# Performance work log

Measured on AMD Instinct MI355X. Metric: run time of the kernel, lower is better.

## Reference

```python
import jax, jax.numpy as jnp
import numpy as np

D_MODEL = 1024
NUM_HEADS = 16
D_K = D_MODEL // NUM_HEADS


def setup_inputs() -> dict:
    key = jax.random.key(0)
    ks = jax.random.split(key, 11)
    B, S, D = 4, 2048, D_MODEL
    scale = 1.0 / np.sqrt(D)
    return {
        "Q": jax.random.normal(ks[0], (B, S, D), jnp.float32),
        "K": jax.random.normal(ks[1], (B, S, D), jnp.float32),
        "V": jax.random.normal(ks[2], (B, S, D), jnp.float32),
        "Wq": jax.random.normal(ks[3], (D, D), jnp.float32) * scale,
        "bq": jnp.zeros((D,), jnp.float32),
        "Wk": jax.random.normal(ks[4], (D, D), jnp.float32) * scale,
        "bk": jnp.zeros((D,), jnp.float32),
        "Wv": jax.random.normal(ks[5], (D, D), jnp.float32) * scale,
        "bv": jnp.zeros((D,), jnp.float32),
        "Wo": jax.random.normal(ks[6], (D, D), jnp.float32) * scale,
        "bo": jnp.zeros((D,), jnp.float32),
    }


def reference(Q, K, V, Wq, bq, Wk, bk, Wv, bv, Wo, bo):
    B, S, D = Q.shape
    H, Dk = NUM_HEADS, D_K
    # projections: [B,S,D] -> [B,H,S,Dk]
    def proj(x, W, b):
        y = jnp.einsum('bsd,de->bse', x, W.T) + b  # torch Linear: x @ W.T + b
        return y.reshape(B, -1, H, Dk).transpose(0, 2, 1, 3)
    q = proj(Q, Wq, bq)
    k = proj(K, Wk, bk)
    v = proj(V, Wv, bv)
    scores = jnp.einsum('bhqd,bhkd->bhqk', q, k) / np.sqrt(Dk)  # [B,H,S,S]
    attn = jax.nn.softmax(scores, axis=-1)
    out = jnp.einsum('bhqk,bhkd->bhqd', attn, v)  # [B,H,S,Dk]
    out = out.transpose(0, 2, 1, 3).reshape(B, -1, D)
    return jnp.einsum('bsd,de->bse', out, Wo.T) + bo
```

## Files before the change

### kernel.cpp

```cpp
#include <hip/hip_runtime.h>


typedef __bf16 bhalf_t;
typedef __attribute__((ext_vector_type(8)))  __bf16 bf16x8;
typedef __attribute__((ext_vector_type(4)))  __bf16 bf16x4;
typedef __attribute__((ext_vector_type(4)))  float  f32x4;
typedef __attribute__((ext_vector_type(16))) float  f32x16;

typedef __attribute__((address_space(1))) void gvoid_t;
typedef __attribute__((address_space(3))) void lvoid_t;
#define GLD16(g, l) __builtin_amdgcn_global_load_lds((const gvoid_t*)(g), (lvoid_t*)(l), 16, 0, 0)

__global__ __launch_bounds__(256) void cvt_all(
    const float* __restrict__ Q, const float* __restrict__ Kin, const float* __restrict__ V,
    const float* __restrict__ Wq, const float* __restrict__ Wk, const float* __restrict__ Wv,
    const float* __restrict__ Wo,
    bhalf_t* __restrict__ Qb, bhalf_t* __restrict__ Kb, bhalf_t* __restrict__ Vb,
    bhalf_t* __restrict__ Wqb, bhalf_t* __restrict__ Wkb, bhalf_t* __restrict__ Wvb,
    bhalf_t* __restrict__ Wob)
{
  size_t t = (size_t)blockIdx.x * 256 + threadIdx.x;
  const float* src; bhalf_t* dst;
  if (t < 2097152)      { src = Q;   dst = Qb; }
  else if (t < 4194304) { src = Kin; dst = Kb; t -= 2097152; }
  else if (t < 6291456) { src = V;   dst = Vb; t -= 4194304; }
  else {
    t -= 6291456;
    int w = (int)(t >> 18); t &= 262143;
    src = (w == 0) ? Wq  : (w == 1) ? Wk  : (w == 2) ? Wv  : Wo;
    dst = (w == 0) ? Wqb : (w == 1) ? Wkb : (w == 2) ? Wvb : Wob;
  }
  float4 f = ((const float4*)src)[t];
  bf16x4 o;
  o.x = (bhalf_t)f.x; o.y = (bhalf_t)f.y; o.z = (bhalf_t)f.z; o.w = (bhalf_t)f.w;
  ((bf16x4*)dst)[t] = o;
}

__device__ __forceinline__ void gemm_core_128_swz(
    const bhalf_t* __restrict__ A, const bhalf_t* __restrict__ B,
    int bm, int bn, bhalf_t* As, bhalf_t* Bs, f32x4 acc[4][4])
{
  const int tid = threadIdx.x, lane = tid & 63, wave = tid >> 6;
  const int wm = wave >> 1, wn = wave & 1;
  const int quad = lane >> 4, tn = lane & 15;

  const int u    = (lane & 7) ^ (lane >> 3);
  const int roff = (lane >> 3) + 64 * (u >> 2);
  const int gk   = (u & 3) * 8;

  const bhalf_t* Ag0 = A + (size_t)(bm * 128 + wave * 8 + roff) * 1024 + gk;
  const bhalf_t* Ag1 = A + (size_t)(bm * 128 + (wave + 4) * 8 + roff) * 1024 + gk;
  const bhalf_t* Bg0 = B + (size_t)(bn * 128 + wave * 8 + roff) * 1024 + gk;
  const bhalf_t* Bg1 = B + (size_t)(bn * 128 + (wave + 4) * 8 + roff) * 1024 + gk;
  bhalf_t* Ad0 = As + wave * 512;  bhalf_t* Ad1 = As + (wave + 4) * 512;
  bhalf_t* Bd0 = Bs + wave * 512;  bhalf_t* Bd1 = Bs + (wave + 4) * 512;

  const int aswz = ((wm * 4 + quad) ^ (tn & 7)) * 8;
  const int bswz = ((wn * 4 + quad) ^ (tn & 7)) * 8;

  for (int k0 = 0; k0 < 1024; k0 += 32) {
    GLD16(Ag0 + k0, Ad0);
    GLD16(Ag1 + k0, Ad1);
    GLD16(Bg0 + k0, Bd0);
    GLD16(Bg1 + k0, Bd1);
    __syncthreads();
    bf16x8 af[4], bfr[4];
#pragma unroll
    for (int i = 0; i < 4; ++i)
      af[i] = *(const bf16x8*)(As + (i * 16 + tn) * 64 + aswz);
#pragma unroll
    for (int j = 0; j < 4; ++j)
      bfr[j] = *(const bf16x8*)(Bs + (j * 16 + tn) * 64 + bswz);
#pragma unroll
    for (int i = 0; i < 4; ++i)
#pragma unroll
      for (int j = 0; j < 4; ++j)
        acc[i][j] = __builtin_amdgcn_mfma_f32_16x16x32_bf16(af[i], bfr[j], acc[i][j], 0, 0, 0);
    __syncthreads();
  }
}

__global__ __launch_bounds__(256) void proj_gemm(
    const bhalf_t* __restrict__ Qb, const bhalf_t* __restrict__ Kb, const bhalf_t* __restrict__ Vb,
    const bhalf_t* __restrict__ Wqb, const bhalf_t* __restrict__ Wkb, const bhalf_t* __restrict__ Wvb,
    const float* __restrict__ bq, const float* __restrict__ bk, const float* __restrict__ bv,
    bhalf_t* __restrict__ qo, bhalf_t* __restrict__ ko, bhalf_t* __restrict__ vto)
{
  __shared__ bhalf_t As[4096];
  __shared__ bhalf_t Bs[4096];
  const int seg = blockIdx.x >> 9;
  const int idx = blockIdx.x & 511;
  const int bm = idx & 63, bn = idx >> 6;

  const bhalf_t *A, *Bw; const float* bias; bhalf_t* out; float scale; int mode;
  if (seg == 0)      { A = Qb; Bw = Wqb; bias = bq; out = qo;  scale = 0.18033688f; mode = 0; }
  else if (seg == 1) { A = Kb; Bw = Wkb; bias = bk; out = ko;  scale = 1.0f;        mode = 0; }
  else               { A = Vb; Bw = Wvb; bias = bv; out = vto; scale = 1.0f;        mode = 1; }

  f32x4 acc[4][4];
#pragma unroll
  for (int i = 0; i < 4; ++i)
#pragma unroll
    for (int j = 0; j < 4; ++j)
      acc[i][j] = (f32x4){0.f, 0.f, 0.f, 0.f};

  gemm_core_128_swz(A, Bw, bm, bn, As, Bs, acc);

  const int lane = threadIdx.x & 63, wave = threadIdx.x >> 6;
  const int wm = wave >> 1, wn = wave & 1, quad = lane >> 4, tn = lane & 15;
#pragma unroll
  for (int i = 0; i < 4; ++i)
#pragma unroll
    for (int j = 0; j < 4; ++j) {
      const int n = bn * 128 + wn * 64 + j * 16 + tn;
      const float bsv = bias[n];
      const int h = n >> 6, dk = n & 63;
#pragma unroll
      for (int r = 0; r < 4; ++r) {
        const int m = bm * 128 + wm * 64 + i * 16 + quad * 4 + r;
        const int b = m >> 11, s = m & 2047;
        const float v = (acc[i][j][r] + bsv) * scale;
        size_t addr;
        if (mode == 0) addr = (((size_t)(b * 16 + h)) * 2048 + s) * 64 + dk;
        else {
          const int s2 = (s & ~12) | ((s & 4) << 1) | ((s & 8) >> 1);
          addr = (((size_t)(b * 16 + h)) * 64 + dk) * 2048 + s2;
        }
        out[addr] = (bhalf_t)v;
      }
    }
}

__global__ __launch_bounds__(256) void out_gemm(
    const bhalf_t* __restrict__ A, const bhalf_t* __restrict__ Bw,
    const float* __restrict__ bias, float* __restrict__ Cout)
{
  __shared__ bhalf_t As[4096];
  __shared__ bhalf_t Bs[4096];
  const int bm = blockIdx.x & 63, bn = blockIdx.x >> 6;

  f32x4 acc[4][4];
#pragma unroll
  for (int i = 0; i < 4; ++i)
#pragma unroll
    for (int j = 0; j < 4; ++j)
      acc[i][j] = (f32x4){0.f, 0.f, 0.f, 0.f};

  gemm_core_128_swz(A, Bw, bm, bn, As, Bs, acc);

  const int lane = threadIdx.x & 63, wave = threadIdx.x >> 6;
  const int wm = wave >> 1, wn = wave & 1, quad = lane >> 4, tn = lane & 15;
#pragma unroll
  for (int i = 0; i < 4; ++i)
#pragma unroll
    for (int j = 0; j < 4; ++j) {
      const int n = bn * 128 + wn * 64 + j * 16 + tn;
      const float bsv = bias[n];
#pragma unroll
      for (int r = 0; r < 4; ++r) {
        const int m = bm * 128 + wm * 64 + i * 16 + quad * 4 + r;
        Cout[(size_t)m * 1024 + n] = acc[i][j][r] + bsv;
      }
    }
}

__global__ __launch_bounds__(256, 2) void attn_kernel(
    const bhalf_t* __restrict__ qp, const bhalf_t* __restrict__ kp,
    const bhalf_t* __restrict__ vtp, bhalf_t* __restrict__ outp)
{
  __shared__ bhalf_t Klds[4096];
  __shared__ bhalf_t Vtlds[4096];

  const int tid = threadIdx.x, lane = tid & 63, wave = tid >> 6;
  const int q31 = lane & 31, h = lane >> 5;
  const int bh = blockIdx.y, qt = blockIdx.x;

  const bhalf_t* qbase = qp + (((size_t)bh * 2048) + qt * 256 + wave * 64 + q31) * 64;
  bf16x8 qf[2][4];
#pragma unroll
  for (int qs = 0; qs < 2; ++qs)
#pragma unroll
    for (int ks = 0; ks < 4; ++ks)
      qf[qs][ks] = *(const bf16x8*)(qbase + qs * 32 * 64 + ks * 16 + h * 8);

  f32x16 Ot[2][2];
#pragma unroll
  for (int qs = 0; qs < 2; ++qs)
#pragma unroll
    for (int dd = 0; dd < 2; ++dd)
#pragma unroll
      for (int i = 0; i < 16; ++i) Ot[qs][dd][i] = 0.f;
  float Lp[2] = {0.f, 0.f};

  const bhalf_t* kbase  = kp  + (size_t)bh * 2048 * 64;
  const bhalf_t* vtbase = vtp + (size_t)bh * 64 * 2048;

  const int rloc = lane >> 3;
  const int cg8  = ((lane & 7) ^ rloc) * 8;
  const int q7 = q31 & 7;

  for (int kv0 = 0; kv0 < 2048; kv0 += 64) {
#pragma unroll
    for (int i = 0; i < 2; ++i) {
      const int r0 = (wave * 2 + i) * 8;
      GLD16(kbase + (size_t)(kv0 + r0 + rloc) * 64 + cg8, Klds + r0 * 64);
      GLD16(vtbase + (size_t)(r0 + rloc) * 2048 + kv0 + cg8, Vtlds + r0 * 64);
    }
    __syncthreads();

    bf16x8 pb[2][4];
#pragma unroll
    for (int mb = 0; mb < 2; ++mb) {
      bf16x8 ka[4];
#pragma unroll
      for (int ks = 0; ks < 4; ++ks)
        ka[ks] = *(const bf16x8*)(Klds + (mb * 32 + q31) * 64 + ((2 * ks + h) ^ q7) * 8);
#pragma unroll
      for (int qs = 0; qs < 2; ++qs) {
        f32x16 S;
#pragma unroll
        for (int i = 0; i < 16; ++i) S[i] = 0.f;
#pragma unroll
        for (int ks = 0; ks < 4; ++ks)
          S = __builtin_amdgcn_mfma_f32_32x32x16_bf16(ka[ks], qf[qs][ks], S, 0, 0, 0);
        float ls = 0.f;
#pragma unroll
        for (int half = 0; half < 2; ++half) {
          bf16x8 pk;
#pragma unroll
          for (int j = 0; j < 8; ++j) {
            const float e = __builtin_amdgcn_exp2f(S[half * 8 + j]);
            ls += e;
            pk[j] = (bhalf_t)e;
          }
          pb[qs][mb * 2 + half] = pk;
        }
        Lp[qs] += ls;
      }
    }

#pragma unroll
    for (int dd = 0; dd < 2; ++dd)
#pragma unroll
      for (int kb = 0; kb < 4; ++kb) {
        const bf16x8 va = *(const bf16x8*)(Vtlds + (dd * 32 + q31) * 64 + ((2 * kb + h) ^ q7) * 8);
#pragma unroll
        for (int qs = 0; qs < 2; ++qs)
          Ot[qs][dd] = __builtin_amdgcn_mfma_f32_32x32x16_bf16(va, pb[qs][kb], Ot[qs][dd], 0, 0, 0);
      }
    __syncthreads();
  }

  const int b = bh >> 4, hh = bh & 15;
#pragma unroll
  for (int qs = 0; qs < 2; ++qs) {
    const float Lt = Lp[qs] + __shfl_xor(Lp[qs], 32, 64);
    const float linv = 1.0f / Lt;
    const int s = qt * 256 + wave * 64 + qs * 32 + q31;
    bhalf_t* ob = outp + ((size_t)(b * 2048 + s)) * 1024 + hh * 64;
#pragma unroll
    for (int dd = 0; dd < 2; ++dd)
#pragma unroll
      for (int g = 0; g < 4; ++g) {
        bf16x4 o;
        o.x = (bhalf_t)(Ot[qs][dd][4 * g + 0] * linv);
        o.y = (bhalf_t)(Ot[qs][dd][4 * g + 1] * linv);
        o.z = (bhalf_t)(Ot[qs][dd][4 * g + 2] * linv);
        o.w = (bhalf_t)(Ot[qs][dd][4 * g + 3] * linv);
        *(bf16x4*)(ob + dd * 32 + g * 8 + h * 4) = o;
      }
  }
}

extern "C" void kernel_launch(void* const* d_in, const int* in_sizes, int n_in,
                              void* d_out, int out_size, void* d_ws, size_t ws_size,
                              hipStream_t stream)
{
  const float* Q  = (const float*)d_in[0];
  const float* K  = (const float*)d_in[1];
  const float* V  = (const float*)d_in[2];
  const float* Wq = (const float*)d_in[3];
  const float* bq = (const float*)d_in[4];
  const float* Wk = (const float*)d_in[5];
  const float* bk = (const float*)d_in[6];
  const float* Wv = (const float*)d_in[7];
  const float* bv = (const float*)d_in[8];
  const float* Wo = (const float*)d_in[9];
  const float* bo = (const float*)d_in[10];

  char* ws = (char*)d_ws;
  const size_t SZ = 8192ull * 1024 * 2;
  const size_t WZ = 1024ull * 1024 * 2;
  bhalf_t* Qb   = (bhalf_t*)(ws);
  bhalf_t* Kb   = (bhalf_t*)(ws + SZ);
  bhalf_t* Vb   = (bhalf_t*)(ws + 2 * SZ);
  bhalf_t* Wqb  = (bhalf_t*)(ws + 3 * SZ);
  bhalf_t* Wkb  = (bhalf_t*)(ws + 3 * SZ + WZ);
  bhalf_t* Wvb  = (bhalf_t*)(ws + 3 * SZ + 2 * WZ);
  bhalf_t* Wob  = (bhalf_t*)(ws + 3 * SZ + 3 * WZ);
  bhalf_t* q_p  = (bhalf_t*)(ws + 3 * SZ + 4 * WZ);
  bhalf_t* k_p  = (bhalf_t*)(ws + 4 * SZ + 4 * WZ);
  bhalf_t* vt_p = (bhalf_t*)(ws + 5 * SZ + 4 * WZ);
  bhalf_t* attn_o = Qb;

  cvt_all<<<28672, 256, 0, stream>>>(Q, K, V, Wq, Wk, Wv, Wo,
                                     Qb, Kb, Vb, Wqb, Wkb, Wvb, Wob);
  proj_gemm<<<1536, 256, 0, stream>>>(Qb, Kb, Vb, Wqb, Wkb, Wvb,
                                      bq, bk, bv, q_p, k_p, vt_p);
  attn_kernel<<<dim3(8, 64), 256, 0, stream>>>(q_p, k_p, vt_p, attn_o);
  out_gemm<<<512, 256, 0, stream>>>(attn_o, Wob, bo, (float*)d_out);
}
```

Measured before the change: 334.8 us.

## Double-buffer attention K/V tiles, widen projection GEMM K-tile, reorder attention grid

The attention kernel now keeps two LDS buffers for K and V^T and prefetches the next 64-key tile while computing on the current one. This removes the barrier wait on loads at the top of every iteration. The projection GEMM is inlined with a 64-wide K step, which halves the number of barrier round trips per tile but doubles its LDS footprint. The attention grid is transposed so that consecutive blocks walk across batch-heads rather than query tiles, which changes L2 locality for K/V. Together these raise LDS use per block, which may affect occupancy.

```diff
diff --git a/kernel.cpp b/kernel.cpp
--- a/kernel.cpp
+++ b/kernel.cpp
@@ -86,8 +86,8 @@
     const float* __restrict__ bq, const float* __restrict__ bk, const float* __restrict__ bv,
     bhalf_t* __restrict__ qo, bhalf_t* __restrict__ ko, bhalf_t* __restrict__ vto)
 {
-  __shared__ bhalf_t As[4096];
-  __shared__ bhalf_t Bs[4096];
+  __shared__ bhalf_t As[8192];
+  __shared__ bhalf_t Bs[8192];
   const int seg = blockIdx.x >> 9;
   const int idx = blockIdx.x & 511;
   const int bm = idx & 63, bn = idx >> 6;
@@ -97,6 +97,19 @@
   else if (seg == 1) { A = Kb; Bw = Wkb; bias = bk; out = ko;  scale = 1.0f;        mode = 0; }
   else               { A = Vb; Bw = Wvb; bias = bv; out = vto; scale = 1.0f;        mode = 1; }
 
+  const int tid = threadIdx.x, lane = tid & 63, wave = tid >> 6;
+  const int wm = wave >> 1, wn = wave & 1;
+  const int quad = lane >> 4, tn = lane & 15;
+  const int u = (lane & 7) ^ (lane >> 3);
+
+  const bhalf_t* Agp[4]; const bhalf_t* Bgp[4];
+#pragma unroll
+  for (int g = 0; g < 4; ++g) {
+    const int row = g * 32 + wave * 8 + (lane >> 3);
+    Agp[g] = A  + (size_t)(bm * 128 + row) * 1024 + u * 8;
+    Bgp[g] = Bw + (size_t)(bn * 128 + row) * 1024 + u * 8;
+  }
+
   f32x4 acc[4][4];
 #pragma unroll
   for (int i = 0; i < 4; ++i)
@@ -104,20 +117,45 @@
     for (int j = 0; j < 4; ++j)
       acc[i][j] = (f32x4){0.f, 0.f, 0.f, 0.f};
 
-  gemm_core_128_swz(A, Bw, bm, bn, As, Bs, acc);
-
-  const int lane = threadIdx.x & 63, wave = threadIdx.x >> 6;
-  const int wm = wave >> 1, wn = wave & 1, quad = lane >> 4, tn = lane & 15;
+  for (int k0 = 0; k0 < 1024; k0 += 64) {
+#pragma unroll
+    for (int g = 0; g < 4; ++g) {
+      GLD16(Agp[g] + k0, As + g * 2048 + wave * 512);
+      GLD16(Bgp[g] + k0, Bs + g * 2048 + wave * 512);
+    }
+    __syncthreads();
+#pragma unroll
+    for (int kk = 0; kk < 2; ++kk) {
+      bf16x8 af[4], bfr[4];
+#pragma unroll
+      for (int i = 0; i < 4; ++i)
+        af[i] = *(const bf16x8*)(As + (wm * 64 + i * 16 + tn) * 64
+                                    + (((kk * 4 + quad) ^ (tn & 7)) * 8));
+#pragma unroll
+      for (int j = 0; j < 4; ++j)
+        bfr[j] = *(const bf16x8*)(Bs + (wn * 64 + j * 16 + tn) * 64
+                                     + (((kk * 4 + quad) ^ (tn & 7)) * 8));
+#pragma unroll
+      for (int i = 0; i < 4; ++i)
+#pragma unroll
+        for (int j = 0; j < 4; ++j)
+          acc[i][j] = __builtin_amdgcn_mfma_f32_16x16x32_bf16(af[i], bfr[j], acc[i][j], 0, 0, 0);
+    }
+    __syncthreads();
+  }
+
+  const int lane2 = threadIdx.x & 63, wave2 = threadIdx.x >> 6;
+  const int wm2 = wave2 >> 1, wn2 = wave2 & 1, quad2 = lane2 >> 4, tn2 = lane2 & 15;
 #pragma unroll
   for (int i = 0; i < 4; ++i)
 #pragma unroll
     for (int j = 0; j < 4; ++j) {
-      const int n = bn * 128 + wn * 64 + j * 16 + tn;
+      const int n = bn * 128 + wn2 * 64 + j * 16 + tn2;
       const float bsv = bias[n];
       const int h = n >> 6, dk = n & 63;
 #pragma unroll
       for (int r = 0; r < 4; ++r) {
-        const int m = bm * 128 + wm * 64 + i * 16 + quad * 4 + r;
+        const int m = bm * 128 + wm2 * 64 + i * 16 + quad2 * 4 + r;
         const int b = m >> 11, s = m & 2047;
         const float v = (acc[i][j][r] + bsv) * scale;
         size_t addr;
@@ -168,12 +206,12 @@
     const bhalf_t* __restrict__ qp, const bhalf_t* __restrict__ kp,
     const bhalf_t* __restrict__ vtp, bhalf_t* __restrict__ outp)
 {
-  __shared__ bhalf_t Klds[4096];
-  __shared__ bhalf_t Vtlds[4096];
+  __shared__ bhalf_t Klds[2][4096];
+  __shared__ bhalf_t Vtlds[2][4096];
 
   const int tid = threadIdx.x, lane = tid & 63, wave = tid >> 6;
   const int q31 = lane & 31, h = lane >> 5;
-  const int bh = blockIdx.y, qt = blockIdx.x;
+  const int bh = blockIdx.x, qt = blockIdx.y;
 
   const bhalf_t* qbase = qp + (((size_t)bh * 2048) + qt * 256 + wave * 64 + q31) * 64;
   bf16x8 qf[2][4];
@@ -199,14 +237,26 @@
   const int cg8  = ((lane & 7) ^ rloc) * 8;
   const int q7 = q31 & 7;
 
+#pragma unroll
+  for (int i = 0; i < 2; ++i) {
+    const int r0 = (wave * 2 + i) * 8;
+    GLD16(kbase + (size_t)(r0 + rloc) * 64 + cg8, &Klds[0][r0 * 64]);
+    GLD16(vtbase + (size_t)(r0 + rloc) * 2048 + cg8, &Vtlds[0][r0 * 64]);
+  }
+  __syncthreads();
+
   for (int kv0 = 0; kv0 < 2048; kv0 += 64) {
-#pragma unroll
-    for (int i = 0; i < 2; ++i) {
-      const int r0 = (wave * 2 + i) * 8;
-      GLD16(kbase + (size_t)(kv0 + r0 + rloc) * 64 + cg8, Klds + r0 * 64);
-      GLD16(vtbase + (size_t)(r0 + rloc) * 2048 + kv0 + cg8, Vtlds + r0 * 64);
-    }
-    __syncthreads();
+    const int cur = (kv0 >> 6) & 1, nxt = cur ^ 1;
+    if (kv0 < 2048 - 64) {
+#pragma unroll
+      for (int i = 0; i < 2; ++i) {
+        const int r0 = (wave * 2 + i) * 8;
+        GLD16(kbase + (size_t)(kv0 + 64 + r0 + rloc) * 64 + cg8, &Klds[nxt][r0 * 64]);
+        GLD16(vtbase + (size_t)(r0 + rloc) * 2048 + (kv0 + 64) + cg8, &Vtlds[nxt][r0 * 64]);
+      }
+    }
+    const bhalf_t* Kc = Klds[cur];
+    const bhalf_t* Vc = Vtlds[cur];
 
     bf16x8 pb[2][4];
 #pragma unroll
@@ -214,7 +264,7 @@
       bf16x8 ka[4];
 #pragma unroll
       for (int ks = 0; ks < 4; ++ks)
-        ka[ks] = *(const bf16x8*)(Klds + (mb * 32 + q31) * 64 + ((2 * ks + h) ^ q7) * 8);
+        ka[ks] = *(const bf16x8*)(Kc + (mb * 32 + q31) * 64 + ((2 * ks + h) ^ q7) * 8);
 #pragma unroll
       for (int qs = 0; qs < 2; ++qs) {
         f32x16 S;
@@ -243,7 +293,7 @@
     for (int dd = 0; dd < 2; ++dd)
 #pragma unroll
       for (int kb = 0; kb < 4; ++kb) {
-        const bf16x8 va = *(const bf16x8*)(Vtlds + (dd * 32 + q31) * 64 + ((2 * kb + h) ^ q7) * 8);
+        const bf16x8 va = *(const bf16x8*)(Vc + (dd * 32 + q31) * 64 + ((2 * kb + h) ^ q7) * 8);
 #pragma unroll
         for (int qs = 0; qs < 2; ++qs)
           Ot[qs][dd] = __builtin_amdgcn_mfma_f32_32x32x16_bf16(va, pb[qs][kb], Ot[qs][dd], 0, 0, 0);
@@ -307,6 +357,6 @@
                                      Qb, Kb, Vb, Wqb, Wkb, Wvb, Wob);
   proj_gemm<<<1536, 256, 0, stream>>>(Qb, Kb, Vb, Wqb, Wkb, Wvb,
                                       bq, bk, bv, q_p, k_p, vt_p);
-  attn_kernel<<<dim3(8, 64), 256, 0, stream>>>(q_p, k_p, vt_p, attn_o);
+  attn_kernel<<<dim3(64, 8), 256, 0, stream>>>(q_p, k_p, vt_p, attn_o);
   out_gemm<<<512, 256, 0, stream>>>(attn_o, Wob, bo, (float*)d_out);
 }
```

Result: no change. 330.4 us (-1.3%).

## Double-buffer K/V tiles in attention and shrink query tile for occupancy

Applied to the files above, without the earlier changes.

The attention kernel now handles 128 queries per block instead of 256, so each wave owns one 32-row query slice and the grid doubles to 1024 blocks, ordered with batch-head as the fast dimension. K and V^T tiles are double-buffered in LDS: the next tile is prefetched with async global-to-LDS loads while the current tile is computed, which leaves one barrier per iteration. Launch bounds go from 2 to 4 blocks per SIMD to raise occupancy and hide latency. In exchange, each K/V tile is reused by half as many queries, so global and L2 traffic for K/V roughly doubles, and LDS use per block doubles.

```diff
diff --git a/kernel.cpp b/kernel.cpp
--- a/kernel.cpp
+++ b/kernel.cpp
@@ -164,33 +164,29 @@
     }
 }
 
-__global__ __launch_bounds__(256, 2) void attn_kernel(
+__global__ __launch_bounds__(256, 4) void attn_kernel(
     const bhalf_t* __restrict__ qp, const bhalf_t* __restrict__ kp,
     const bhalf_t* __restrict__ vtp, bhalf_t* __restrict__ outp)
 {
-  __shared__ bhalf_t Klds[4096];
-  __shared__ bhalf_t Vtlds[4096];
+  __shared__ bhalf_t Klds[2][4096];
+  __shared__ bhalf_t Vtlds[2][4096];
 
   const int tid = threadIdx.x, lane = tid & 63, wave = tid >> 6;
   const int q31 = lane & 31, h = lane >> 5;
-  const int bh = blockIdx.y, qt = blockIdx.x;
-
-  const bhalf_t* qbase = qp + (((size_t)bh * 2048) + qt * 256 + wave * 64 + q31) * 64;
-  bf16x8 qf[2][4];
-#pragma unroll
-  for (int qs = 0; qs < 2; ++qs)
-#pragma unroll
-    for (int ks = 0; ks < 4; ++ks)
-      qf[qs][ks] = *(const bf16x8*)(qbase + qs * 32 * 64 + ks * 16 + h * 8);
-
-  f32x16 Ot[2][2];
-#pragma unroll
-  for (int qs = 0; qs < 2; ++qs)
-#pragma unroll
-    for (int dd = 0; dd < 2; ++dd)
-#pragma unroll
-      for (int i = 0; i < 16; ++i) Ot[qs][dd][i] = 0.f;
-  float Lp[2] = {0.f, 0.f};
+  const int bh = blockIdx.x, qt = blockIdx.y;
+
+  const bhalf_t* qbase = qp + (((size_t)bh * 2048) + qt * 128 + wave * 32 + q31) * 64;
+  bf16x8 qf[4];
+#pragma unroll
+  for (int ks = 0; ks < 4; ++ks)
+    qf[ks] = *(const bf16x8*)(qbase + ks * 16 + h * 8);
+
+  f32x16 Ot[2];
+#pragma unroll
+  for (int dd = 0; dd < 2; ++dd)
+#pragma unroll
+    for (int i = 0; i < 16; ++i) Ot[dd][i] = 0.f;
+  float Lp = 0.f;
 
   const bhalf_t* kbase  = kp  + (size_t)bh * 2048 * 64;
   const bhalf_t* vtbase = vtp + (size_t)bh * 64 * 2048;
@@ -199,77 +195,81 @@
   const int cg8  = ((lane & 7) ^ rloc) * 8;
   const int q7 = q31 & 7;
 
+#pragma unroll
+  for (int i = 0; i < 2; ++i) {
+    const int r0 = (wave * 2 + i) * 8;
+    GLD16(kbase + (size_t)(r0 + rloc) * 64 + cg8, &Klds[0][r0 * 64]);
+    GLD16(vtbase + (size_t)(r0 + rloc) * 2048 + cg8, &Vtlds[0][r0 * 64]);
+  }
+  __syncthreads();
+
   for (int kv0 = 0; kv0 < 2048; kv0 += 64) {
-#pragma unroll
-    for (int i = 0; i < 2; ++i) {
-      const int r0 = (wave * 2 + i) * 8;
-      GLD16(kbase + (size_t)(kv0 + r0 + rloc) * 64 + cg8, Klds + r0 * 64);
-      GLD16(vtbase + (size_t)(r0 + rloc) * 2048 + kv0 + cg8, Vtlds + r0 * 64);
-    }
-    __syncthreads();
-
-    bf16x8 pb[2][4];
+    const int cur = (kv0 >> 6) & 1, nxt = cur ^ 1;
+    if (kv0 < 2048 - 64) {
+#pragma unroll
+      for (int i = 0; i < 2; ++i) {
+        const int r0 = (wave * 2 + i) * 8;
+        GLD16(kbase + (size_t)(kv0 + 64 + r0 + rloc) * 64 + cg8, &Klds[nxt][r0 * 64]);
+        GLD16(vtbase + (size_t)(r0 + rloc) * 2048 + (kv0 + 64) + cg8, &Vtlds[nxt][r0 * 64]);
+      }
+    }
+    const bhalf_t* Kc = Klds[cur];
+    const bhalf_t* Vc = Vtlds[cur];
+
+    bf16x8 pb[4];
 #pragma unroll
     for (int mb = 0; mb < 2; ++mb) {
       bf16x8 ka[4];
 #pragma unroll
       for (int ks = 0; ks < 4; ++ks)
-        ka[ks] = *(const bf16x8*)(Klds + (mb * 32 + q31) * 64 + ((2 * ks + h) ^ q7) * 8);
-#pragma unroll
-      for (int qs = 0; qs < 2; ++qs) {
-        f32x16 S;
-#pragma unroll
-        for (int i = 0; i < 16; ++i) S[i] = 0.f;
-#pragma unroll
-        for (int ks = 0; ks < 4; ++ks)
-          S = __builtin_amdgcn_mfma_f32_32x32x16_bf16(ka[ks], qf[qs][ks], S, 0, 0, 0);
-        float ls = 0.f;
-#pragma unroll
-        for (int half = 0; half < 2; ++half) {
-          bf16x8 pk;
-#pragma unroll
-          for (int j = 0; j < 8; ++j) {
-            const float e = __builtin_amdgcn_exp2f(S[half * 8 + j]);
-            ls += e;
-            pk[j] = (bhalf_t)e;
-          }
-          pb[qs][mb * 2 + half] = pk;
+        ka[ks] = *(const bf16x8*)(Kc + (mb * 32 + q31) * 64 + ((2 * ks + h) ^ q7) * 8);
+      f32x16 S;
+#pragma unroll
+      for (int i = 0; i < 16; ++i) S[i] = 0.f;
+#pragma unroll
+      for (int ks = 0; ks < 4; ++ks)
+        S = __builtin_amdgcn_mfma_f32_32x32x16_bf16(ka[ks], qf[ks], S, 0, 0, 0);
+      float ls = 0.f;
+#pragma unroll
+      for (int half = 0; half < 2; ++half) {
+        bf16x8 pk;
+#pragma unroll
+        for (int j = 0; j < 8; ++j) {
+          const float e = __builtin_amdgcn_exp2f(S[half * 8 + j]);
+          ls += e;
+          pk[j] = (bhalf_t)e;
         }
-        Lp[qs] += ls;
-      }
+        pb[mb * 2 + half] = pk;
+      }
+      Lp += ls;
     }
 
 #pragma unroll
     for (int dd = 0; dd < 2; ++dd)
 #pragma unroll
       for (int kb = 0; kb < 4; ++kb) {
-        const bf16x8 va = *(const bf16x8*)(Vtlds + (dd * 32 + q31) * 64 + ((2 * kb + h) ^ q7) * 8);
-#pragma unroll
-        for (int qs = 0; qs < 2; ++qs)
-          Ot[qs][dd] = __builtin_amdgcn_mfma_f32_32x32x16_bf16(va, pb[qs][kb], Ot[qs][dd], 0, 0, 0);
+        const bf16x8 va = *(const bf16x8*)(Vc + (dd * 32 + q31) * 64 + ((2 * kb + h) ^ q7) * 8);
+        Ot[dd] = __builtin_amdgcn_mfma_f32_32x32x16_bf16(va, pb[kb], Ot[dd], 0, 0, 0);
       }
     __syncthreads();
   }
 
   const int b = bh >> 4, hh = bh & 15;
-#pragma unroll
-  for (int qs = 0; qs < 2; ++qs) {
-    const float Lt = Lp[qs] + __shfl_xor(Lp[qs], 32, 64);
-    const float linv = 1.0f / Lt;
-    const int s = qt * 256 + wave * 64 + qs * 32 + q31;
-    bhalf_t* ob = outp + ((size_t)(b * 2048 + s)) * 1024 + hh * 64;
-#pragma unroll
-    for (int dd = 0; dd < 2; ++dd)
-#pragma unroll
-      for (int g = 0; g < 4; ++g) {
-        bf16x4 o;
-        o.x = (bhalf_t)(Ot[qs][dd][4 * g + 0] * linv);
-        o.y = (bhalf_t)(Ot[qs][dd][4 * g + 1] * linv);
-        o.z = (bhalf_t)(Ot[qs][dd][4 * g + 2] * linv);
-        o.w = (bhalf_t)(Ot[qs][dd][4 * g + 3] * linv);
-        *(bf16x4*)(ob + dd * 32 + g * 8 + h * 4) = o;
-      }
-  }
+  const float Lt = Lp + __shfl_xor(Lp, 32, 64);
+  const float linv = 1.0f / Lt;
+  const int s = qt * 128 + wave * 32 + q31;
+  bhalf_t* ob = outp + ((size_t)(b * 2048 + s)) * 1024 + hh * 64;
+#pragma unroll
+  for (int dd = 0; dd < 2; ++dd)
+#pragma unroll
+    for (int g = 0; g < 4; ++g) {
+      bf16x4 o;
+      o.x = (bhalf_t)(Ot[dd][4 * g + 0] * linv);
+      o.y = (bhalf_t)(Ot[dd][4 * g + 1] * linv);
+      o.z = (bhalf_t)(Ot[dd][4 * g + 2] * linv);
+      o.w = (bhalf_t)(Ot[dd][4 * g + 3] * linv);
+      *(bf16x4*)(ob + dd * 32 + g * 8 + h * 4) = o;
+    }
 }
 
 extern "C" void kernel_launch(void* const* d_in, const int* in_sizes, int n_in,
@@ -307,6 +307,6 @@
                                      Qb, Kb, Vb, Wqb, Wkb, Wvb, Wob);
   proj_gemm<<<1536, 256, 0, stream>>>(Qb, Kb, Vb, Wqb, Wkb, Wvb,
                                       bq, bk, bv, q_p, k_p, vt_p);
-  attn_kernel<<<dim3(8, 64), 256, 0, stream>>>(q_p, k_p, vt_p, attn_o);
+  attn_kernel<<<dim3(64, 16), 256, 0, stream>>>(q_p, k_p, vt_p, attn_o);
   out_gemm<<<512, 256, 0, stream>>>(attn_o, Wob, bo, (float*)d_out);
 }
```

After: 344.1 us. 2.8% more time.
